# Optimization experiments

Hardware: AMD Instinct MI355X
Metric: run time of the kernel (lower is better)

The kernel has to match this reference:

```python
import jax, jax.numpy as jnp
import numpy as np

N_NODES = 50000
NEG_SLOPE = 0.2

def _gat_conv(x, W, att_src, att_dst, bias, src, dst):
    # x: [N, in_c] -> h: [N, out_c]
    h = x @ W
    a_src = (h * att_src).sum(-1)  # [N]
    a_dst = (h * att_dst).sum(-1)  # [N]
    e = a_src[src] + a_dst[dst]    # [E]
    e = jnp.where(e > 0, e, NEG_SLOPE * e)  # LeakyReLU
    # segment softmax over destination node neighborhoods
    emax = jax.ops.segment_max(e, dst, num_segments=N_NODES)
    ee = jnp.exp(e - emax[dst])
    denom = jax.ops.segment_sum(ee, dst, num_segments=N_NODES)
    alpha = ee / denom[dst]        # [E]
    out = jax.ops.segment_sum(h[src] * alpha[:, None], dst, num_segments=N_NODES)
    return out + bias

def _with_self_loops(edge_index):
    # PyG GATConv default add_self_loops=True
    loop = jnp.arange(N_NODES, dtype=edge_index.dtype)
    src = jnp.concatenate([edge_index[0], loop])
    dst = jnp.concatenate([edge_index[1], loop])
    return src, dst

def setup_inputs() -> dict:
    key = jax.random.key(0)
    ks = jax.random.split(key, 11)
    in_c, hid_c, out_c = 256, 128, 64
    E = 800000
    x = jax.random.normal(ks[0], (N_NODES, in_c), dtype=jnp.float32)
    edge_index = jax.random.randint(ks[1], (2, E), 0, N_NODES, dtype=jnp.int64)
    s1 = 1.0 / np.sqrt(in_c)
    s2 = 1.0 / np.sqrt(hid_c)
    return {
        "x": x,
        "edge_index": edge_index,
        "W1": jax.random.normal(ks[2], (in_c, hid_c), dtype=jnp.float32) * s1,
        "att_src1": jax.random.normal(ks[3], (hid_c,), dtype=jnp.float32) * s2,
        "att_dst1": jax.random.normal(ks[4], (hid_c,), dtype=jnp.float32) * s2,
        "b1": jax.random.normal(ks[5], (hid_c,), dtype=jnp.float32) * 0.01,
        "W2": jax.random.normal(ks[6], (hid_c, out_c), dtype=jnp.float32) * s2,
        "att_src2": jax.random.normal(ks[7], (out_c,), dtype=jnp.float32) * (1.0 / np.sqrt(out_c)),
        "att_dst2": jax.random.normal(ks[8], (out_c,), dtype=jnp.float32) * (1.0 / np.sqrt(out_c)),
        "b2": jax.random.normal(ks[9], (out_c,), dtype=jnp.float32) * 0.01,
    }

def reference(x, edge_index, W1, att_src1, att_dst1, b1, W2, att_src2, att_dst2, b2):
    src, dst = _with_self_loops(edge_index)
    hid = _gat_conv(x, W1, att_src1, att_dst1, b1, src, dst)
    hid = jax.nn.relu(hid)
    out = _gat_conv(hid, W2, att_src2, att_dst2, b2, src, dst)
    return jax.nn.log_softmax(out, axis=1)
```

## Files before the change

kernel.cpp:

```cpp
#include <hip/hip_runtime.h>
#include <hip/hip_bf16.h>
#include <math.h>

#define N_NODES 50000
#define E_RAW   800000
#define E_TOT   850000
#define NEG_SLOPE 0.2f
#define CAP 64

#define NBKT   392
#define BCAP   2944
#define SCHUNK 4096
#define SB     208

typedef __attribute__((ext_vector_type(8))) short short8;
typedef __attribute__((ext_vector_type(4))) float f32x4;
typedef __attribute__((ext_vector_type(4))) unsigned short ushort4_t;

__device__ __forceinline__ short f2bf(float f) {
    __hip_bfloat16 h = __float2bfloat16(f);
    return *reinterpret_cast<short*>(&h);
}
__device__ __forceinline__ unsigned int f2bfu(float f) {
    __hip_bfloat16 h = __float2bfloat16(f);
    return (unsigned int)*reinterpret_cast<unsigned short*>(&h);
}
__device__ __forceinline__ float bflo(unsigned int u) {
    return __uint_as_float(u << 16);
}
__device__ __forceinline__ float bfhi(unsigned int u) {
    return __uint_as_float(u & 0xffff0000u);
}

template<int K, int N>
__global__ __launch_bounds__(256) void gat_wf_kernel(
        const float* __restrict__ W, short* __restrict__ Wf) {
    constexpr int NT = N / 16;
    const int idx = blockIdx.x * 256 + threadIdx.x;
    if (idx >= K * N) return;
    const int j  = idx & 7;
    const int n  = (idx >> 3) & 15;
    const int q  = (idx >> 7) & 3;
    const int t  = (idx >> 9) % NT;
    const int kc = idx / (512 * NT);
    const int k   = kc * 32 + q * 8 + j;
    const int col = t * 16 + n;
    Wf[idx] = f2bf(W[(size_t)k * N + col]);
}

template<int K, int N, bool BF16_IN>
__device__ __forceinline__ void gemm_att_body(
        const int blk,
        const float* __restrict__ xf, const short* __restrict__ xb,
        const short* __restrict__ Wf,
        const float* __restrict__ att_src, const float* __restrict__ att_dst,
        short* __restrict__ h_bf,
        float* __restrict__ a_src, float* __restrict__ a_dst) {
    constexpr int NT = N / 16;
    constexpr int KC = K / 32;
    const int tid  = threadIdx.x;
    const int lane = tid & 63;
    const int wv   = tid >> 6;
    const int mrow = lane & 15;
    const int q    = lane >> 4;

    const int row0 = blk * 64 + wv * 16;
    const int rowA = row0 + mrow;
    const int rowAc = rowA < N_NODES ? rowA : 0;

    f32x4 acc[NT];
    #pragma unroll
    for (int t = 0; t < NT; ++t) acc[t] = f32x4{0.f, 0.f, 0.f, 0.f};

    #pragma unroll
    for (int kc = 0; kc < KC; ++kc) {
        short8 a;
        if (BF16_IN) {
            a = *(const short8*)&xb[(size_t)rowAc * K + kc * 32 + q * 8];
        } else {
            const float4 f0 = *(const float4*)&xf[(size_t)rowAc * K + kc * 32 + q * 8];
            const float4 f1 = *(const float4*)&xf[(size_t)rowAc * K + kc * 32 + q * 8 + 4];
            a[0] = f2bf(f0.x); a[1] = f2bf(f0.y); a[2] = f2bf(f0.z); a[3] = f2bf(f0.w);
            a[4] = f2bf(f1.x); a[5] = f2bf(f1.y); a[6] = f2bf(f1.z); a[7] = f2bf(f1.w);
        }
        #pragma unroll
        for (int t = 0; t < NT; ++t) {
            const short8 b = *(const short8*)&Wf[((size_t)(kc * NT + t) * 64 + lane) * 8];
            acc[t] = __builtin_amdgcn_mfma_f32_16x16x32_bf16(a, b, acc[t], 0, 0, 0);
        }
    }

    #pragma unroll
    for (int r = 0; r < 4; ++r) {
        const int rowD = row0 + q * 4 + r;
        float ps = 0.0f, pd = 0.0f;
        #pragma unroll
        for (int t = 0; t < NT; ++t) {
            const int col = t * 16 + mrow;
            ps = fmaf(acc[t][r], att_src[col], ps);
            pd = fmaf(acc[t][r], att_dst[col], pd);
        }
        #pragma unroll
        for (int off = 8; off > 0; off >>= 1) {
            ps += __shfl_xor(ps, off);
            pd += __shfl_xor(pd, off);
        }
        if (rowD < N_NODES) {
            if (mrow == 0) { a_src[rowD] = ps; a_dst[rowD] = pd; }
            #pragma unroll
            for (int t = 0; t < NT; ++t)
                h_bf[(size_t)rowD * N + t * 16 + mrow] = f2bf(acc[t][r]);
        }
    }
}

template<int K, int N>
__global__ __launch_bounds__(256) void gat_fat1_kernel(
        const float* __restrict__ xf, const short* __restrict__ Wf,
        const float* __restrict__ att_src, const float* __restrict__ att_dst,
        short* __restrict__ h_bf,
        float* __restrict__ a_src, float* __restrict__ a_dst,
        const int* __restrict__ ei, int* __restrict__ gcnt,
        unsigned int* __restrict__ buf, int GB) {
    __shared__ int hist[NBKT];
    __shared__ int base[NBKT];
    if ((int)blockIdx.x < GB) {
        gemm_att_body<K, N, false>(blockIdx.x, xf, nullptr, Wf,
                                   att_src, att_dst, h_bf, a_src, a_dst);
    } else {
        const int sb = (int)blockIdx.x - GB;
        const int c0 = sb * SCHUNK;
        const int c1 = (c0 + SCHUNK < E_TOT) ? c0 + SCHUNK : E_TOT;
        for (int t = threadIdx.x; t < NBKT; t += 256) hist[t] = 0;
        __syncthreads();
        for (int i = c0 + threadIdx.x; i < c1; i += 256) {
            const int d = (i < E_RAW) ? ei[E_RAW + i] : (i - E_RAW);
            atomicAdd(&hist[d >> 7], 1);
        }
        __syncthreads();
        for (int t = threadIdx.x; t < NBKT; t += 256)
            base[t] = atomicAdd(&gcnt[t], hist[t]);
        __syncthreads();
        for (int t = threadIdx.x; t < NBKT; t += 256) hist[t] = 0;
        __syncthreads();
        for (int i = c0 + threadIdx.x; i < c1; i += 256) {
            int s, d;
            if (i < E_RAW) { s = ei[i]; d = ei[E_RAW + i]; }
            else           { s = d = i - E_RAW; }
            const int b = d >> 7;
            const int p = base[b] + atomicAdd(&hist[b], 1);
            if (p < BCAP)
                buf[(size_t)b * BCAP + p] =
                    ((unsigned int)s << 7) | (unsigned int)(d & 127);
        }
    }
}

__global__ __launch_bounds__(256) void gat_ell_kernel(
        const unsigned int* __restrict__ buf, const int* __restrict__ gcnt,
        int* __restrict__ cnt, unsigned short* __restrict__ srcs) {
    const int b = blockIdx.x;
    __shared__ unsigned int c2[128];
    if (threadIdx.x < 128) c2[threadIdx.x] = 0;
    __syncthreads();
    int n = gcnt[b];
    n = n < BCAP ? n : BCAP;
    const unsigned int* bb = buf + (size_t)b * BCAP;
    for (int i = threadIdx.x; i < n; i += 256) {
        const unsigned int e = bb[i];
        const int dl = (int)(e & 127u);
        const unsigned int s = e >> 7;
        const unsigned int c = atomicAdd(&c2[dl], 1u);
        if (c < CAP)
            srcs[((size_t)((b << 7) + dl) << 6) + c] = (unsigned short)s;
    }
    __syncthreads();
    const int d = (b << 7) + threadIdx.x;
    if (threadIdx.x < 128 && d < N_NODES) {
        unsigned int c = c2[threadIdx.x];
        cnt[d] = (int)(c < CAP ? c : CAP);
    }
}

template<int K, int N, bool BF16_IN>
__global__ __launch_bounds__(256) void gat_gemm_att_kernel(
        const float* __restrict__ xf, const short* __restrict__ xb,
        const short* __restrict__ Wf,
        const float* __restrict__ att_src, const float* __restrict__ att_dst,
        short* __restrict__ h_bf,
        float* __restrict__ a_src, float* __restrict__ a_dst) {
    gemm_att_body<K, N, BF16_IN>(blockIdx.x, xf, xb, Wf,
                                 att_src, att_dst, h_bf, a_src, a_dst);
}

template<int N, bool RELU, bool LSM>
__global__ __launch_bounds__(256) void gat_aggr_kernel(
        const int* __restrict__ cnt, const unsigned short* __restrict__ srcs,
        const float* __restrict__ a_src, const float* __restrict__ a_dst,
        const unsigned short* __restrict__ h_bf, const float* __restrict__ bias,
        float* __restrict__ outf, uint4* __restrict__ outb) {
    constexpr int EPL = N / 16;
    __shared__ __align__(16) float lalpha[1024];
    __shared__ __align__(8)  unsigned short lsrc[1024];
    __shared__ int   ldeg[16];
    __shared__ float ladst[16];
    const int tid = threadIdx.x;
    const int d0 = blockIdx.x * 16;

    if (tid < 16) {
        const int d = d0 + tid;
        int dg = cnt[d];
        ldeg[tid]  = dg < CAP ? dg : CAP;
        ladst[tid] = a_dst[d];
    }
    __syncthreads();

    {
        const int dl = tid >> 4;
        const int so = (tid & 15) * 4;
        const int dg = ldeg[dl];
        const float ad = ladst[dl];
        const ushort4_t s4 =
            *(const ushort4_t*)(srcs + ((size_t)(d0 + dl) << 6) + so);
        float e[4];
        #pragma unroll
        for (int i = 0; i < 4; ++i) {
            if (so + i < dg) {
                const float t = a_src[(int)s4[i]] + ad;
                e[i] = t > 0.0f ? t : NEG_SLOPE * t;
            } else {
                e[i] = -1e30f;
            }
        }
        float m = fmaxf(fmaxf(e[0], e[1]), fmaxf(e[2], e[3]));
        #pragma unroll
        for (int off = 1; off < 16; off <<= 1) m = fmaxf(m, __shfl_xor(m, off));
        float ex[4], ss = 0.0f;
        #pragma unroll
        for (int i = 0; i < 4; ++i) { ex[i] = __expf(e[i] - m); ss += ex[i]; }
        #pragma unroll
        for (int off = 1; off < 16; off <<= 1) ss += __shfl_xor(ss, off);
        const float rinv = 1.0f / ss;
        float4 av;
        av.x = ex[0] * rinv; av.y = ex[1] * rinv;
        av.z = ex[2] * rinv; av.w = ex[3] * rinv;
        *(float4*)&lalpha[(dl << 6) + so] = av;
        *(ushort4_t*)&lsrc[(dl << 6) + so] = s4;
    }
    __syncthreads();

    const int lane = tid & 63;
    const int g    = lane >> 4;
    const int sub  = lane & 15;
    const int dl   = (tid >> 6) * 4 + g;
    const int d    = d0 + dl;
    const int deg  = ldeg[dl];
    const int base = dl << 6;

    float acc[EPL];
    #pragma unroll
    for (int c = 0; c < EPL; ++c) acc[c] = 0.0f;

    int j = 0;
    for (; j + 2 <= deg; j += 2) {
        const int s0   = (int)lsrc[base + j];
        const int s1   = (int)lsrc[base + j + 1];
        const float al0 = lalpha[base + j];
        const float al1 = lalpha[base + j + 1];
        const unsigned short* hp0 = h_bf + (size_t)s0 * N + sub * EPL;
        const unsigned short* hp1 = h_bf + (size_t)s1 * N + sub * EPL;
        if (EPL == 8) {
            const uint4 h0 = *(const uint4*)hp0;
            const uint4 h1 = *(const uint4*)hp1;
            acc[0] = fmaf(al0, bflo(h0.x), acc[0]);
            acc[1] = fmaf(al0, bfhi(h0.x), acc[1]);
            acc[2] = fmaf(al0, bflo(h0.y), acc[2]);
            acc[3] = fmaf(al0, bfhi(h0.y), acc[3]);
            acc[4] = fmaf(al0, bflo(h0.z), acc[4]);
            acc[5] = fmaf(al0, bfhi(h0.z), acc[5]);
            acc[6] = fmaf(al0, bflo(h0.w), acc[6]);
            acc[7] = fmaf(al0, bfhi(h0.w), acc[7]);
            acc[0] = fmaf(al1, bflo(h1.x), acc[0]);
            acc[1] = fmaf(al1, bfhi(h1.x), acc[1]);
            acc[2] = fmaf(al1, bflo(h1.y), acc[2]);
            acc[3] = fmaf(al1, bfhi(h1.y), acc[3]);
            acc[4] = fmaf(al1, bflo(h1.z), acc[4]);
            acc[5] = fmaf(al1, bfhi(h1.z), acc[5]);
            acc[6] = fmaf(al1, bflo(h1.w), acc[6]);
            acc[7] = fmaf(al1, bfhi(h1.w), acc[7]);
        } else {
            const uint2 h0 = *(const uint2*)hp0;
            const uint2 h1 = *(const uint2*)hp1;
            acc[0] = fmaf(al0, bflo(h0.x), acc[0]);
            acc[1] = fmaf(al0, bfhi(h0.x), acc[1]);
            acc[2] = fmaf(al0, bflo(h0.y), acc[2]);
            acc[3] = fmaf(al0, bfhi(h0.y), acc[3]);
            acc[0] = fmaf(al1, bflo(h1.x), acc[0]);
            acc[1] = fmaf(al1, bfhi(h1.x), acc[1]);
            acc[2] = fmaf(al1, bflo(h1.y), acc[2]);
            acc[3] = fmaf(al1, bfhi(h1.y), acc[3]);
        }
    }
    if (j < deg) {
        const int s0    = (int)lsrc[base + j];
        const float al0 = lalpha[base + j];
        const unsigned short* hp0 = h_bf + (size_t)s0 * N + sub * EPL;
        if (EPL == 8) {
            const uint4 h0 = *(const uint4*)hp0;
            acc[0] = fmaf(al0, bflo(h0.x), acc[0]);
            acc[1] = fmaf(al0, bfhi(h0.x), acc[1]);
            acc[2] = fmaf(al0, bflo(h0.y), acc[2]);
            acc[3] = fmaf(al0, bfhi(h0.y), acc[3]);
            acc[4] = fmaf(al0, bflo(h0.z), acc[4]);
            acc[5] = fmaf(al0, bfhi(h0.z), acc[5]);
            acc[6] = fmaf(al0, bflo(h0.w), acc[6]);
            acc[7] = fmaf(al0, bfhi(h0.w), acc[7]);
        } else {
            const uint2 h0 = *(const uint2*)hp0;
            acc[0] = fmaf(al0, bflo(h0.x), acc[0]);
            acc[1] = fmaf(al0, bfhi(h0.x), acc[1]);
            acc[2] = fmaf(al0, bflo(h0.y), acc[2]);
            acc[3] = fmaf(al0, bfhi(h0.y), acc[3]);
        }
    }

    if (LSM) {
        float v[4];
        #pragma unroll
        for (int c = 0; c < 4; ++c) v[c] = acc[c] + bias[sub * 4 + c];
        float mm = fmaxf(fmaxf(v[0], v[1]), fmaxf(v[2], v[3]));
        #pragma unroll
        for (int off = 1; off < 16; off <<= 1) mm = fmaxf(mm, __shfl_xor(mm, off));
        float es = __expf(v[0] - mm) + __expf(v[1] - mm)
                 + __expf(v[2] - mm) + __expf(v[3] - mm);
        #pragma unroll
        for (int off = 1; off < 16; off <<= 1) es += __shfl_xor(es, off);
        const float ls = logf(es);
        float4 o;
        o.x = v[0] - mm - ls; o.y = v[1] - mm - ls;
        o.z = v[2] - mm - ls; o.w = v[3] - mm - ls;
        *(float4*)&outf[(size_t)d * N + sub * 4] = o;
    } else {
        const float4 b0 = *(const float4*)&bias[sub * 8];
        const float4 b1 = *(const float4*)&bias[sub * 8 + 4];
        float v[8];
        v[0] = acc[0] + b0.x; v[1] = acc[1] + b0.y;
        v[2] = acc[2] + b0.z; v[3] = acc[3] + b0.w;
        v[4] = acc[4] + b1.x; v[5] = acc[5] + b1.y;
        v[6] = acc[6] + b1.z; v[7] = acc[7] + b1.w;
        if (RELU)
            #pragma unroll
            for (int c = 0; c < 8; ++c) v[c] = fmaxf(v[c], 0.0f);
        uint4 p;
        p.x = f2bfu(v[0]) | (f2bfu(v[1]) << 16);
        p.y = f2bfu(v[2]) | (f2bfu(v[3]) << 16);
        p.z = f2bfu(v[4]) | (f2bfu(v[5]) << 16);
        p.w = f2bfu(v[6]) | (f2bfu(v[7]) << 16);
        outb[(size_t)d * (N / 8) + sub] = p;
    }
}

extern "C" void kernel_launch(void* const* d_in, const int* in_sizes, int n_in,
                              void* d_out, int out_size, void* d_ws, size_t ws_size,
                              hipStream_t stream) {
    const float* x        = (const float*)d_in[0];
    const int*   ei       = (const int*)  d_in[1];
    const float* W1       = (const float*)d_in[2];
    const float* att_src1 = (const float*)d_in[3];
    const float* att_dst1 = (const float*)d_in[4];
    const float* b1       = (const float*)d_in[5];
    const float* W2       = (const float*)d_in[6];
    const float* att_src2 = (const float*)d_in[7];
    const float* att_dst2 = (const float*)d_in[8];
    const float* b2       = (const float*)d_in[9];
    float* out = (float*)d_out;
    float* ws  = (float*)d_ws;

    float* a_src1 = ws;
    float* a_dst1 = a_src1 + 50000;
    float* a_src2 = a_dst1 + 50000;
    float* a_dst2 = a_src2 + 50000;
    int*   cnt    = (int*)(a_dst2 + 50000);
    int*   gcnt   = cnt + 50000;
    unsigned int*   buf  = (unsigned int*)(gcnt + 512);
    unsigned short* srcs = (unsigned short*)(buf + (size_t)NBKT * BCAP);
    short* hbf1   = (short*)(srcs + (size_t)N_NODES * CAP);
    short* agg1b  = hbf1  + 6400000;
    short* Wf1    = agg1b + 6400000;
    short* Wf2    = Wf1   + 32768;
    short* hbf2   = hbf1;

    hipMemsetAsync(gcnt, 0, NBKT * sizeof(int), stream);

    const int GB = (N_NODES + 63) / 64;

    gat_wf_kernel<256, 128><<<128, 256, 0, stream>>>(W1, Wf1);
    gat_wf_kernel<128, 64><<<32, 256, 0, stream>>>(W2, Wf2);

    gat_fat1_kernel<256, 128><<<GB + SB, 256, 0, stream>>>(
        x, Wf1, att_src1, att_dst1, hbf1, a_src1, a_dst1,
        ei, gcnt, buf, GB);

    gat_ell_kernel<<<NBKT, 256, 0, stream>>>(buf, gcnt, cnt, srcs);

    gat_aggr_kernel<128, true, false><<<3125, 256, 0, stream>>>(
        cnt, srcs, a_src1, a_dst1, (const unsigned short*)hbf1, b1,
        nullptr, (uint4*)agg1b);

    gat_gemm_att_kernel<128, 64, true><<<GB, 256, 0, stream>>>(
        nullptr, agg1b, Wf2, att_src2, att_dst2, hbf2, a_src2, a_dst2);
    gat_aggr_kernel<64, false, true><<<3125, 256, 0, stream>>>(
        cnt, srcs, a_src2, a_dst2, (const unsigned short*)hbf2, b2,
        out, nullptr);
}
```

Baseline: 209.5 us.

## Fuse layer-1 aggregation with layer-2 GEMM and attention projection

Layer-1 neighbourhood aggregation (bias, ReLU, bf16 pack) now writes its 16-node tile into shared memory, and the same block runs the 128x64 layer-2 projection with MFMA plus the attention dot products. This removes the intermediate agg1 buffer round-trip through global memory and one kernel launch. hbf2 gets its own buffer because hbf1 is still being read by other blocks. In exchange the aggregation kernel uses more shared memory and registers, and the tiny per-block GEMM reloads W2 from global in every block.

```diff
diff --git a/kernel.cpp b/kernel.cpp
--- a/kernel.cpp
+++ b/kernel.cpp
@@ -182,15 +182,166 @@
     }
 }
 
-template<int K, int N, bool BF16_IN>
-__global__ __launch_bounds__(256) void gat_gemm_att_kernel(
-        const float* __restrict__ xf, const short* __restrict__ xb,
-        const short* __restrict__ Wf,
-        const float* __restrict__ att_src, const float* __restrict__ att_dst,
-        short* __restrict__ h_bf,
-        float* __restrict__ a_src, float* __restrict__ a_dst) {
-    gemm_att_body<K, N, BF16_IN>(blockIdx.x, xf, xb, Wf,
-                                 att_src, att_dst, h_bf, a_src, a_dst);
+__global__ __launch_bounds__(256) void gat_aggr1_fused_kernel(
+        const int* __restrict__ cnt, const unsigned short* __restrict__ srcs,
+        const float* __restrict__ a_src, const float* __restrict__ a_dst,
+        const unsigned short* __restrict__ h_bf, const float* __restrict__ bias,
+        const short* __restrict__ Wf2,
+        const float* __restrict__ att_src2, const float* __restrict__ att_dst2,
+        short* __restrict__ hbf2,
+        float* __restrict__ a_src2, float* __restrict__ a_dst2) {
+    constexpr int N = 128;
+    __shared__ __align__(16) float lalpha[1024];
+    __shared__ __align__(8)  unsigned short lsrc[1024];
+    __shared__ int   ldeg[16];
+    __shared__ float ladst[16];
+    __shared__ __align__(16) short lh[16 * 136];
+    __shared__ float pspart[64], pdpart[64];
+    const int tid = threadIdx.x;
+    const int d0 = blockIdx.x * 16;
+
+    if (tid < 16) {
+        const int d = d0 + tid;
+        int dg = cnt[d];
+        ldeg[tid]  = dg < CAP ? dg : CAP;
+        ladst[tid] = a_dst[d];
+    }
+    __syncthreads();
+
+    {
+        const int dl = tid >> 4;
+        const int so = (tid & 15) * 4;
+        const int dg = ldeg[dl];
+        const float ad = ladst[dl];
+        const ushort4_t s4 =
+            *(const ushort4_t*)(srcs + ((size_t)(d0 + dl) << 6) + so);
+        float e[4];
+        #pragma unroll
+        for (int i = 0; i < 4; ++i) {
+            if (so + i < dg) {
+                const float t = a_src[(int)s4[i]] + ad;
+                e[i] = t > 0.0f ? t : NEG_SLOPE * t;
+            } else {
+                e[i] = -1e30f;
+            }
+        }
+        float m = fmaxf(fmaxf(e[0], e[1]), fmaxf(e[2], e[3]));
+        #pragma unroll
+        for (int off = 1; off < 16; off <<= 1) m = fmaxf(m, __shfl_xor(m, off));
+        float ex[4], ss = 0.0f;
+        #pragma unroll
+        for (int i = 0; i < 4; ++i) { ex[i] = __expf(e[i] - m); ss += ex[i]; }
+        #pragma unroll
+        for (int off = 1; off < 16; off <<= 1) ss += __shfl_xor(ss, off);
+        const float rinv = 1.0f / ss;
+        float4 av;
+        av.x = ex[0] * rinv; av.y = ex[1] * rinv;
+        av.z = ex[2] * rinv; av.w = ex[3] * rinv;
+        *(float4*)&lalpha[(dl << 6) + so] = av;
+        *(ushort4_t*)&lsrc[(dl << 6) + so] = s4;
+    }
+    __syncthreads();
+
+    const int lane = tid & 63;
+    const int g    = lane >> 4;
+    const int sub  = lane & 15;
+    const int dl   = (tid >> 6) * 4 + g;
+    const int deg  = ldeg[dl];
+    const int base = dl << 6;
+
+    float acc[8];
+    #pragma unroll
+    for (int c = 0; c < 8; ++c) acc[c] = 0.0f;
+
+    int j = 0;
+    for (; j + 2 <= deg; j += 2) {
+        const int s0   = (int)lsrc[base + j];
+        const int s1   = (int)lsrc[base + j + 1];
+        const float al0 = lalpha[base + j];
+        const float al1 = lalpha[base + j + 1];
+        const uint4 h0 = *(const uint4*)(h_bf + (size_t)s0 * N + sub * 8);
+        const uint4 h1 = *(const uint4*)(h_bf + (size_t)s1 * N + sub * 8);
+        acc[0] = fmaf(al0, bflo(h0.x), acc[0]);
+        acc[1] = fmaf(al0, bfhi(h0.x), acc[1]);
+        acc[2] = fmaf(al0, bflo(h0.y), acc[2]);
+        acc[3] = fmaf(al0, bfhi(h0.y), acc[3]);
+        acc[4] = fmaf(al0, bflo(h0.z), acc[4]);
+        acc[5] = fmaf(al0, bfhi(h0.z), acc[5]);
+        acc[6] = fmaf(al0, bflo(h0.w), acc[6]);
+        acc[7] = fmaf(al0, bfhi(h0.w), acc[7]);
+        acc[0] = fmaf(al1, bflo(h1.x), acc[0]);
+        acc[1] = fmaf(al1, bfhi(h1.x), acc[1]);
+        acc[2] = fmaf(al1, bflo(h1.y), acc[2]);
+        acc[3] = fmaf(al1, bfhi(h1.y), acc[3]);
+        acc[4] = fmaf(al1, bflo(h1.z), acc[4]);
+        acc[5] = fmaf(al1, bfhi(h1.z), acc[5]);
+        acc[6] = fmaf(al1, bflo(h1.w), acc[6]);
+        acc[7] = fmaf(al1, bfhi(h1.w), acc[7]);
+    }
+    if (j < deg) {
+        const int s0    = (int)lsrc[base + j];
+        const float al0 = lalpha[base + j];
+        const uint4 h0 = *(const uint4*)(h_bf + (size_t)s0 * N + sub * 8);
+        acc[0] = fmaf(al0, bflo(h0.x), acc[0]);
+        acc[1] = fmaf(al0, bfhi(h0.x), acc[1]);
+        acc[2] = fmaf(al0, bflo(h0.y), acc[2]);
+        acc[3] = fmaf(al0, bfhi(h0.y), acc[3]);
+        acc[4] = fmaf(al0, bflo(h0.z), acc[4]);
+        acc[5] = fmaf(al0, bfhi(h0.z), acc[5]);
+        acc[6] = fmaf(al0, bflo(h0.w), acc[6]);
+        acc[7] = fmaf(al0, bfhi(h0.w), acc[7]);
+    }
+
+    {
+        const float4 b0 = *(const float4*)&bias[sub * 8];
+        const float4 b1 = *(const float4*)&bias[sub * 8 + 4];
+        float v[8];
+        v[0] = fmaxf(acc[0] + b0.x, 0.0f); v[1] = fmaxf(acc[1] + b0.y, 0.0f);
+        v[2] = fmaxf(acc[2] + b0.z, 0.0f); v[3] = fmaxf(acc[3] + b0.w, 0.0f);
+        v[4] = fmaxf(acc[4] + b1.x, 0.0f); v[5] = fmaxf(acc[5] + b1.y, 0.0f);
+        v[6] = fmaxf(acc[6] + b1.z, 0.0f); v[7] = fmaxf(acc[7] + b1.w, 0.0f);
+        uint4 p;
+        p.x = f2bfu(v[0]) | (f2bfu(v[1]) << 16);
+        p.y = f2bfu(v[2]) | (f2bfu(v[3]) << 16);
+        p.z = f2bfu(v[4]) | (f2bfu(v[5]) << 16);
+        p.w = f2bfu(v[6]) | (f2bfu(v[7]) << 16);
+        *(uint4*)&lh[dl * 136 + sub * 8] = p;
+    }
+    __syncthreads();
+
+    const int w    = tid >> 6;
+    const int q    = lane >> 4;
+    const int mrow = lane & 15;
+    f32x4 acc2 = f32x4{0.f, 0.f, 0.f, 0.f};
+    #pragma unroll
+    for (int kc = 0; kc < 4; ++kc) {
+        const short8 a = *(const short8*)&lh[mrow * 136 + q * 8 + kc * 32];
+        const short8 b = *(const short8*)&Wf2[((size_t)(kc * 4 + w) * 64 + lane) * 8];
+        acc2 = __builtin_amdgcn_mfma_f32_16x16x32_bf16(a, b, acc2, 0, 0, 0);
+    }
+
+    const float as2 = att_src2[w * 16 + mrow];
+    const float ad2 = att_dst2[w * 16 + mrow];
+    #pragma unroll
+    for (int r = 0; r < 4; ++r) {
+        const int rl = q * 4 + r;
+        float ps = acc2[r] * as2;
+        float pd = acc2[r] * ad2;
+        #pragma unroll
+        for (int off = 1; off < 16; off <<= 1) {
+            ps += __shfl_xor(ps, off);
+            pd += __shfl_xor(pd, off);
+        }
+        if (mrow == 0) { pspart[w * 16 + rl] = ps; pdpart[w * 16 + rl] = pd; }
+        hbf2[(size_t)(d0 + rl) * 64 + w * 16 + mrow] = f2bf(acc2[r]);
+    }
+    __syncthreads();
+    if (tid < 16) {
+        a_src2[d0 + tid] = pspart[tid] + pspart[16 + tid]
+                         + pspart[32 + tid] + pspart[48 + tid];
+        a_dst2[d0 + tid] = pdpart[tid] + pdpart[16 + tid]
+                         + pdpart[32 + tid] + pdpart[48 + tid];
+    }
 }
 
 template<int N, bool RELU, bool LSM>
@@ -385,10 +536,9 @@
     unsigned int*   buf  = (unsigned int*)(gcnt + 512);
     unsigned short* srcs = (unsigned short*)(buf + (size_t)NBKT * BCAP);
     short* hbf1   = (short*)(srcs + (size_t)N_NODES * CAP);
-    short* agg1b  = hbf1  + 6400000;
-    short* Wf1    = agg1b + 6400000;
+    short* hbf2   = hbf1  + 6400000;
+    short* Wf1    = hbf2  + 3200000;
     short* Wf2    = Wf1   + 32768;
-    short* hbf2   = hbf1;
 
     hipMemsetAsync(gcnt, 0, NBKT * sizeof(int), stream);
 
@@ -403,12 +553,10 @@
 
     gat_ell_kernel<<<NBKT, 256, 0, stream>>>(buf, gcnt, cnt, srcs);
 
-    gat_aggr_kernel<128, true, false><<<3125, 256, 0, stream>>>(
+    gat_aggr1_fused_kernel<<<3125, 256, 0, stream>>>(
         cnt, srcs, a_src1, a_dst1, (const unsigned short*)hbf1, b1,
-        nullptr, (uint4*)agg1b);
-
-    gat_gemm_att_kernel<128, 64, true><<<GB, 256, 0, stream>>>(
-        nullptr, agg1b, Wf2, att_src2, att_dst2, hbf2, a_src2, a_dst2);
+        Wf2, att_src2, att_dst2, hbf2, a_src2, a_dst2);
+
     gat_aggr_kernel<64, false, true><<<3125, 256, 0, stream>>>(
         cnt, srcs, a_src2, a_dst2, (const unsigned short*)hbf2, b2,
         out, nullptr);
```

New measurement: 202.4 us. 3.4% less time.
